# Performance work log

Measured on AMD Instinct MI355X. Metric: run time of the kernel, lower is better.

## Reference

```python
import jax, jax.numpy as jnp
import numpy as np

B = 5                      # dat_sz hardcoded in module; kernel shapes force batch == 5
X_DIM = 4096
H_DIM = 4096
T_DIM = 4096
D_DIM = X_DIM // T_DIM     # = 1 (required so z_dim == t_dim broadcasts in reparameterize_nm)
L_DIM = D_DIM * (D_DIM + 1) // 2
Z_DIM = T_DIM * L_DIM      # = 4096


def _linear_params(key, din, dout):
    kw, kb = jax.random.split(key)
    W = jax.random.normal(kw, (din, dout), dtype=jnp.float32) / np.float32(np.sqrt(din))
    b = jax.random.normal(kb, (dout,), dtype=jnp.float32) * np.float32(0.01)
    return W, b


def setup_inputs() -> dict:
    key = jax.random.key(0)
    ks = jax.random.split(key, 20)
    inp = {}
    inp["x"] = jax.random.normal(ks[0], (B, X_DIM), dtype=jnp.float32)
    inp["eps_xi"] = jax.random.normal(ks[1], (B, T_DIM), dtype=jnp.float32)
    inp["eps_f"] = jax.random.normal(ks[2], (B, D_DIM), dtype=jnp.float32)
    inp["eps_z"] = jax.random.normal(ks[3], (B, Z_DIM), dtype=jnp.float32)
    inp["W1"], inp["b1"] = _linear_params(ks[4], X_DIM, H_DIM)
    inp["W11"], inp["b11"] = _linear_params(ks[5], H_DIM, T_DIM)
    inp["W12"], inp["b12"] = _linear_params(ks[6], H_DIM, T_DIM)
    inp["W2"], inp["b2"] = _linear_params(ks[7], D_DIM, H_DIM)
    inp["W21"], inp["b21"] = _linear_params(ks[8], H_DIM, Z_DIM)
    inp["W22"], inp["b22"] = _linear_params(ks[9], H_DIM, T_DIM)
    inp["W23"], inp["b23"] = _linear_params(ks[10], X_DIM + Z_DIM, H_DIM)
    inp["W24"], inp["b24"] = _linear_params(ks[11], H_DIM, T_DIM + D_DIM)
    inp["W25"], inp["b25"] = _linear_params(ks[12], H_DIM, T_DIM + D_DIM)
    inp["W3"], inp["b3"] = _linear_params(ks[13], Z_DIM, H_DIM)
    inp["W31"], inp["b31"] = _linear_params(ks[14], H_DIM, X_DIM)
    inp["W32"], inp["b32"] = _linear_params(ks[15], H_DIM, X_DIM)
    inp["s"] = jax.random.normal(ks[16], (B, T_DIM), dtype=jnp.float32)
    inp["t"] = jax.random.normal(ks[17], (B, D_DIM), dtype=jnp.float32)
    inp["sigma"] = jnp.asarray(0.01, dtype=jnp.float32)
    inp["w"] = jnp.ones((T_DIM,), dtype=jnp.float32) / np.float32(T_DIM)
    inp["dist"] = 1  # unused by forward (matches torch signature)
    return inp


def _ard_kernel(a, b, sigma, w):
    # K[i,j] = sigma^2 * exp(-0.5 * sum_d w_d (a_i,d - b_j,d)^2)
    # Vectorized replacement of the original O(B^2) Python double loop.
    d2 = (a[:, None, :] - b[None, :, :]) ** 2            # [B, B, T]
    return (sigma ** 2) * jnp.exp(-0.5 * jnp.einsum('ijt,t->ij', d2, w))


def reference(x, eps_xi, eps_f, eps_z,
              W1, b1, W11, b11, W12, b12,
              W2, b2, W21, b21, W22, b22,
              W23, b23, W24, b24, W25, b25,
              W3, b3, W31, b31, W32, b32,
              s, t, sigma, w, dist):
    relu = jax.nn.relu
    # encode_1
    h1 = relu(x @ W1 + b1)
    qxi_mean = h1 @ W11 + b11
    log_qxi_cov = h1 @ W12 + b12
    # reparameterize_nm
    xi = jnp.exp(0.5 * log_qxi_cov) * eps_xi + qxi_mean
    # reparameterize_gp (training branch)
    K_ss = _ard_kernel(s, s, sigma, w)                    # [5,5]
    K_xs = _ard_kernel(xi, s, sigma, w)                   # [5,5]
    kk_inv = K_xs @ jnp.linalg.inv(K_ss)                  # [5,5]
    qf_mean = kk_inv @ t                                  # [5,D]
    cov = _ard_kernel(xi, xi, sigma, w) - kk_inv @ _ard_kernel(s, xi, sigma, w)
    qf_cov = jnp.diag(cov)                                # [5]
    f = jnp.sqrt(qf_cov)[:, None] * eps_f + qf_mean       # [5,D]
    # encode_2
    h2 = relu(f @ W2 + b2)
    z_mean = h2 @ W21 + b21                               # [5,Z]
    z_cov = h2 @ W22 + b22                                # [5,T] (== Z since d_dim=1)
    z = jnp.exp(0.5 * z_cov) * eps_z + z_mean
    # encode_3
    h23 = relu(jnp.concatenate([x, z], axis=1) @ W23 + b23)
    r_mean = h23 @ W24 + b24                              # [5,T+D]
    r_cov = h23 @ W25 + b25
    # decode
    h3 = relu(z @ W3 + b3)
    x_mean = h3 @ W31 + b31
    x_cov = h3 @ W32 + b32
    # losses
    qf_cov2 = jnp.broadcast_to(qf_cov[:, None], (B, D_DIM))
    q_mean = jnp.concatenate([qxi_mean, qf_mean], axis=1)
    q_cov = jnp.concatenate([log_qxi_cov, jnp.log(qf_cov2)], axis=1)
    kld1 = 0.5 * jnp.sum(-z_cov - 1.0 + jnp.exp(z_cov) + z_mean ** 2) / B
    kld2 = 0.5 * jnp.sum(r_cov - q_cov - 1.0
                         + jnp.exp(q_cov - r_cov)
                         + (q_mean - r_mean) ** 2 * jnp.exp(-r_cov)) / B
    kld_loss = kld1 + kld2
    log_pi = jnp.log(jnp.asarray(np.pi, dtype=jnp.float32))
    nll_loss = 0.5 * jnp.sum(log_pi + x_cov + jnp.exp(-x_cov) * (x - x_mean) ** 2) / B
    return (kld_loss, nll_loss, z_mean, z_cov, x_mean, x_cov)
```

## Files before the change

kernel.cpp:

```cpp
#include <hip/hip_runtime.h>
#include <math.h>

#define B5 5
#define DX 4096
#define DT 4096
#define DR 4097

enum {
  WS_SUMS  = 0,
  WS_CNT1  = 3,
  WS_CNT2  = 4,
  WS_ZERO_END = 8,
  WS_QXI_F = 16,
  WS_LQC_F = WS_QXI_F + 20480,
  WS_XIV   = WS_LQC_F + 20480,
  WS_Z     = WS_XIV   + 20480,
  WS_KSS   = WS_Z     + 20480,
  WS_KXS   = WS_KSS + 32,
  WS_F     = WS_KXS + 32,
  WS_QFM   = WS_F   + 8,
  WS_QFC   = WS_QFM + 8,
  WS_PART  = 82032,
  WS_P_H1  = WS_PART,
  WS_P_QXI = WS_P_H1  + 1310720,
  WS_P_LQC = WS_P_QXI + 1310720,
  WS_P_ZM  = WS_P_LQC + 1310720,
  WS_P_ZC  = WS_P_ZM  + 1310720,
  WS_P_H23 = WS_P_ZC  + 1310720,
  WS_P_H3  = WS_P_H23 + 2621440,
  WS_P_RM  = WS_P_H3  + 1310720,
  WS_P_RC  = WS_P_RM  + 1311040,
  WS_P_XM  = WS_P_RC  + 1311040,
  WS_P_XC  = WS_P_XM  + 1310720,
  WS_END   = WS_P_XC  + 1310720
};

#define GROWS  64
#define GBLOCK 256

__device__ inline float wave_sum(float v) {
  #pragma unroll
  for (int o = 32; o > 0; o >>= 1) v += __shfl_down(v, o, 64);
  return v;
}

__global__ void k_zero(float* __restrict__ ws)
{
  if (threadIdx.x < WS_ZERO_END) ws[threadIdx.x] = 0.f;
}

template<int PROLOG, int DUAL, int ALIGNED, int NS>
__device__ __forceinline__ void gemm5_body(
    float sx[B5][GROWS], int bx, int by,
    const float* __restrict__ p0, const float* __restrict__ p1,
    const float* __restrict__ p2,
    const float* __restrict__ Wa, const float* __restrict__ Wb,
    float* __restrict__ Pa,       float* __restrict__ Pb,
    int din, int dout)
{
  const int tid = threadIdx.x;
  const long i0 = (long)by * GROWS;

  for (int t = tid; t < B5 * GROWS; t += GBLOCK) {
    int b  = t / GROWS;
    int il = t % GROWS;
    int i  = (int)i0 + il;
    float v;
    if (PROLOG == 0)      v = p0[(long)b * din + i];
    else if (PROLOG == 2) v = fmaxf(p0[b] * p1[i] + p2[i], 0.f);
    else if (PROLOG == 3) v = (i < DX) ? p0[(long)b * DX + i] : p1[(long)b * DT + (i - DX)];
    else {
      const float* pp = p0 + (long)b * din + i;
      float acc = 0.f;
      #pragma unroll 8
      for (int ks = 0; ks < NS; ++ks) acc += pp[(long)ks * (B5 * din)];
      v = fmaxf(acc + p1[i], 0.f);
    }
    sx[b][il] = v;
  }
  __syncthreads();

  long o0 = ((long)bx * GBLOCK + tid) * 2;
  if (o0 >= dout) return;
  const bool has2 = (o0 + 1 < dout);

  float accA[B5][2] = {};
  float accB[B5][2] = {};

  const float* wa = Wa + i0 * dout + o0;
  const float* wb = DUAL ? (Wb + i0 * dout + o0) : nullptr;

  #pragma unroll 4
  for (int il = 0; il < GROWS; ++il) {
    float w0a, w1a, w0b = 0.f, w1b = 0.f;
    if (ALIGNED) {
      float2 ta = *(const float2*)wa; w0a = ta.x; w1a = ta.y;
      if (DUAL) { float2 tb = *(const float2*)wb; w0b = tb.x; w1b = tb.y; }
    } else {
      w0a = wa[0]; w1a = has2 ? wa[1] : 0.f;
      if (DUAL) { w0b = wb[0]; w1b = has2 ? wb[1] : 0.f; }
    }
    #pragma unroll
    for (int b = 0; b < B5; ++b) {
      float xv = sx[b][il];
      accA[b][0] += xv * w0a; accA[b][1] += xv * w1a;
      if (DUAL) { accB[b][0] += xv * w0b; accB[b][1] += xv * w1b; }
    }
    wa += dout; if (DUAL) wb += dout;
  }

  #pragma unroll
  for (int b = 0; b < B5; ++b) {
    float* pa = Pa + ((long)by * B5 + b) * dout + o0;
    if (ALIGNED) *(float2*)pa = make_float2(accA[b][0], accA[b][1]);
    else { pa[0] = accA[b][0]; if (has2) pa[1] = accA[b][1]; }
    if (DUAL) {
      float* pb = Pb + ((long)by * B5 + b) * dout + o0;
      if (ALIGNED) *(float2*)pb = make_float2(accB[b][0], accB[b][1]);
      else { pb[0] = accB[b][0]; if (has2) pb[1] = accB[b][1]; }
    }
  }
}

template<int PROLOG, int DUAL, int ALIGNED, int NS>
__global__ __launch_bounds__(GBLOCK) void gemm5(
    const float* __restrict__ p0, const float* __restrict__ p1,
    const float* __restrict__ p2,
    const float* __restrict__ Wa, const float* __restrict__ Wb,
    float* __restrict__ Pa,       float* __restrict__ Pb,
    int din, int dout)
{
  __shared__ float sx[B5][GROWS];
  gemm5_body<PROLOG, DUAL, ALIGNED, NS>(sx, blockIdx.x, blockIdx.y,
      p0, p1, p2, Wa, Wb, Pa, Pb, din, dout);
}

__global__ __launch_bounds__(256) void k_xi(
    const float* __restrict__ Pq, const float* __restrict__ Pl,
    const float* __restrict__ b11, const float* __restrict__ b12,
    const float* __restrict__ eps_xi,
    float* __restrict__ qf, float* __restrict__ lf, float* __restrict__ xiv)
{
  int idx = blockIdx.x * 256 + threadIdx.x;
  if (idx >= B5 * DT) return;
  int b = idx >> 12, col = idx & (DT - 1);
  const float* pq = Pq + (long)b * DT + col;
  const float* pl = Pl + (long)b * DT + col;
  float sq = 0.f, sl = 0.f;
  #pragma unroll 8
  for (int ks = 0; ks < 64; ++ks) { sq += pq[(long)ks * (B5 * DT)]; sl += pl[(long)ks * (B5 * DT)]; }
  float qm = sq + b11[col];
  float lq = sl + b12[col];
  qf[idx] = qm; lf[idx] = lq;
  xiv[idx] = expf(0.5f * lq) * eps_xi[idx] + qm;
}

__global__ __launch_bounds__(256) void k_ardgp(
    const float* __restrict__ s,    const float* __restrict__ xiv,
    const float* __restrict__ w,    const float* __restrict__ sigma,
    const float* __restrict__ t_in, const float* __restrict__ eps_f,
    float* __restrict__ Kss, float* __restrict__ Kxs, int* __restrict__ cnt,
    float* __restrict__ fv, float* __restrict__ qfm, float* __restrict__ qfc)
{
  const int bid = blockIdx.x;
  const bool xs = (bid >= 25);
  int q = xs ? bid - 25 : bid;
  const int i = q / 5, j = q % 5;
  const float* aa = xs ? (xiv + (long)i * DT) : (s + (long)i * DT);
  const float* bb = s + (long)j * DT;

  float sum = 0.f;
  for (int t = threadIdx.x; t < DT; t += 256) {
    float d = aa[t] - bb[t];
    sum += w[t] * d * d;
  }
  sum = wave_sum(sum);
  __shared__ float red[4];
  int lane = threadIdx.x & 63, wv = threadIdx.x >> 6;
  if (lane == 0) red[wv] = sum;
  __syncthreads();

  if (threadIdx.x == 0) {
    float tot = red[0] + red[1] + red[2] + red[3];
    float sg = sigma[0];
    float K = sg * sg * expf(-0.5f * tot);
    (xs ? Kxs : Kss)[i * 5 + j] = K;
    __threadfence();
    int old = atomicAdd(cnt, 1);
    if (old == 49) {
      __threadfence();
      double M[5][5], Inv[5][5];
      for (int a = 0; a < 5; ++a)
        for (int b = 0; b < 5; ++b) { M[a][b] = Kss[a * 5 + b]; Inv[a][b] = (a == b) ? 1.0 : 0.0; }
      for (int c = 0; c < 5; ++c) {
        int p = c; double best = fabs(M[c][c]);
        for (int r = c + 1; r < 5; ++r) if (fabs(M[r][c]) > best) { best = fabs(M[r][c]); p = r; }
        if (p != c)
          for (int k = 0; k < 5; ++k) {
            double tm = M[c][k]; M[c][k] = M[p][k]; M[p][k] = tm;
            tm = Inv[c][k]; Inv[c][k] = Inv[p][k]; Inv[p][k] = tm;
          }
        double piv = 1.0 / M[c][c];
        for (int k = 0; k < 5; ++k) { M[c][k] *= piv; Inv[c][k] *= piv; }
        for (int r = 0; r < 5; ++r) if (r != c) {
          double m = M[r][c];
          for (int k = 0; k < 5; ++k) { M[r][k] -= m * M[c][k]; Inv[r][k] -= m * Inv[c][k]; }
        }
      }
      double kk[5][5];
      for (int a = 0; a < 5; ++a)
        for (int b = 0; b < 5; ++b) {
          double acc = 0.0;
          for (int k = 0; k < 5; ++k) acc += (double)Kxs[a * 5 + k] * Inv[k][b];
          kk[a][b] = acc;
        }
      double sg2 = (double)sg * (double)sg;
      for (int a = 0; a < 5; ++a) {
        double qm = 0.0, qc = sg2;
        for (int b = 0; b < 5; ++b) { qm += kk[a][b] * (double)t_in[b]; qc -= kk[a][b] * (double)Kxs[a * 5 + b]; }
        if (qc < 1e-12) qc = 1e-12;
        qfm[a] = (float)qm;
        qfc[a] = (float)qc;
        fv[a]  = sqrtf((float)qc) * eps_f[a] + (float)qm;
      }
    }
  }
}

__global__ __launch_bounds__(256) void k_z(
    const float* __restrict__ Pm, const float* __restrict__ Pc,
    const float* __restrict__ b21, const float* __restrict__ b22,
    const float* __restrict__ eps_z,
    float* __restrict__ out_zm, float* __restrict__ out_zc,
    float* __restrict__ zv, float* __restrict__ kld1sum)
{
  int idx = blockIdx.x * 256 + threadIdx.x;
  float term = 0.f;
  if (idx < B5 * DT) {
    int b = idx >> 12, col = idx & (DT - 1);
    const float* pm = Pm + (long)b * DT + col;
    const float* pc = Pc + (long)b * DT + col;
    float sm = 0.f, sc = 0.f;
    #pragma unroll 8
    for (int ks = 0; ks < 64; ++ks) { sm += pm[(long)ks * (B5 * DT)]; sc += pc[(long)ks * (B5 * DT)]; }
    float zm = sm + b21[col];
    float zc = sc + b22[col];
    out_zm[idx] = zm; out_zc[idx] = zc;
    zv[idx] = expf(0.5f * zc) * eps_z[idx] + zm;
    term = -zc - 1.f + expf(zc) + zm * zm;
  }
  term = wave_sum(term);
  if ((threadIdx.x & 63) == 0) atomicAdd(kld1sum, term);
}

__global__ __launch_bounds__(256) void k_fin(
    const float* __restrict__ Prm, const float* __restrict__ Prc,
    const float* __restrict__ b24, const float* __restrict__ b25,
    const float* __restrict__ qxi, const float* __restrict__ lqc,
    const float* __restrict__ qfm, const float* __restrict__ qfc,
    const float* __restrict__ Pxm, const float* __restrict__ Pxc,
    const float* __restrict__ b31, const float* __restrict__ b32,
    const float* __restrict__ x,
    float* __restrict__ out_xm, float* __restrict__ out_xc,
    float* __restrict__ sums, int* __restrict__ cnt, float* __restrict__ out01)
{
  const int gtid = blockIdx.x * 256 + threadIdx.x;
  float t2 = 0.f, t3 = 0.f;
  if (gtid < B5 * DR) {
    int b = gtid / DR, col = gtid % DR;
    const float* pm = Prm + (long)b * DR + col;
    const float* pc = Prc + (long)b * DR + col;
    float sm = 0.f, sc = 0.f;
    #pragma unroll 8
    for (int ks = 0; ks < 64; ++ks) { sm += pm[(long)ks * (B5 * DR)]; sc += pc[(long)ks * (B5 * DR)]; }
    float rm = sm + b24[col];
    float rc = sc + b25[col];
    float qm, qc;
    if (col < DT) { qm = qxi[(long)b * DT + col]; qc = lqc[(long)b * DT + col]; }
    else          { qm = qfm[b]; qc = logf(qfc[b]); }
    float d = qm - rm;
    t2 = rc - qc - 1.f + expf(qc - rc) + d * d * expf(-rc);
  } else {
    int idx = gtid - B5 * DR;
    if (idx < B5 * DX) {
      int b = idx >> 12, col = idx & (DX - 1);
      const float* pm = Pxm + (long)b * DX + col;
      const float* pc = Pxc + (long)b * DX + col;
      float sm = 0.f, sc = 0.f;
      #pragma unroll 8
      for (int ks = 0; ks < 64; ++ks) { sm += pm[(long)ks * (B5 * DX)]; sc += pc[(long)ks * (B5 * DX)]; }
      float xm = sm + b31[col];
      float xc = sc + b32[col];
      out_xm[idx] = xm; out_xc[idx] = xc;
      float d = x[idx] - xm;
      t3 = 1.14472988584940017f + xc + expf(-xc) * d * d;
    }
  }
  t2 = wave_sum(t2);
  t3 = wave_sum(t3);
  if ((threadIdx.x & 63) == 0) {
    if (t2 != 0.f) atomicAdd(&sums[1], t2);
    if (t3 != 0.f) atomicAdd(&sums[2], t3);
  }
  __syncthreads();
  if (threadIdx.x == 0) {
    __threadfence();
    int old = atomicAdd(cnt, 1);
    if (old == (int)gridDim.x - 1) {
      __threadfence();
      out01[0] = 0.5f * (sums[0] + sums[1]) / (float)B5;
      out01[1] = 0.5f * sums[2] / (float)B5;
    }
  }
}

extern "C" void kernel_launch(void* const* d_in, const int* in_sizes, int n_in,
                              void* d_out, int out_size, void* d_ws, size_t ws_size,
                              hipStream_t stream)
{
  const float* x      = (const float*)d_in[0];
  const float* eps_xi = (const float*)d_in[1];
  const float* eps_f  = (const float*)d_in[2];
  const float* eps_z  = (const float*)d_in[3];
  const float* W1  = (const float*)d_in[4];  const float* b1  = (const float*)d_in[5];
  const float* W11 = (const float*)d_in[6];  const float* b11 = (const float*)d_in[7];
  const float* W12 = (const float*)d_in[8];  const float* b12 = (const float*)d_in[9];
  const float* W2  = (const float*)d_in[10]; const float* b2  = (const float*)d_in[11];
  const float* W21 = (const float*)d_in[12]; const float* b21 = (const float*)d_in[13];
  const float* W22 = (const float*)d_in[14]; const float* b22 = (const float*)d_in[15];
  const float* W23 = (const float*)d_in[16]; const float* b23 = (const float*)d_in[17];
  const float* W24 = (const float*)d_in[18]; const float* b24 = (const float*)d_in[19];
  const float* W25 = (const float*)d_in[20]; const float* b25 = (const float*)d_in[21];
  const float* W3  = (const float*)d_in[22]; const float* b3  = (const float*)d_in[23];
  const float* W31 = (const float*)d_in[24]; const float* b31 = (const float*)d_in[25];
  const float* W32 = (const float*)d_in[26]; const float* b32 = (const float*)d_in[27];
  const float* s     = (const float*)d_in[28];
  const float* t     = (const float*)d_in[29];
  const float* sigma = (const float*)d_in[30];
  const float* w     = (const float*)d_in[31];

  float* ws  = (float*)d_ws;
  float* out = (float*)d_out;

  dim3 blk(256);

  k_zero<<<1, 64, 0, stream>>>(ws);

  gemm5<0,0,1,1><<<dim3(8,64), blk, 0, stream>>>(
      x, nullptr, nullptr, W1, nullptr, ws + WS_P_H1, nullptr, 4096, 4096);
  gemm5<4,1,1,64><<<dim3(8,64), blk, 0, stream>>>(
      ws + WS_P_H1, b1, nullptr, W11, W12, ws + WS_P_QXI, ws + WS_P_LQC, 4096, 4096);
  k_xi<<<80, blk, 0, stream>>>(
      ws + WS_P_QXI, ws + WS_P_LQC, b11, b12, eps_xi,
      ws + WS_QXI_F, ws + WS_LQC_F, ws + WS_XIV);
  k_ardgp<<<50, blk, 0, stream>>>(
      s, ws + WS_XIV, w, sigma, t, eps_f,
      ws + WS_KSS, ws + WS_KXS, (int*)(ws + WS_CNT1),
      ws + WS_F, ws + WS_QFM, ws + WS_QFC);
  gemm5<2,1,1,1><<<dim3(8,64), blk, 0, stream>>>(
      ws + WS_F, W2, b2, W21, W22, ws + WS_P_ZM, ws + WS_P_ZC, 4096, 4096);
  k_z<<<80, blk, 0, stream>>>(
      ws + WS_P_ZM, ws + WS_P_ZC, b21, b22, eps_z,
      out + 2, out + 2 + 20480, ws + WS_Z, ws + WS_SUMS);
  gemm5<3,0,1,1><<<dim3(8,128), blk, 0, stream>>>(
      x, ws + WS_Z, nullptr, W23, nullptr, ws + WS_P_H23, nullptr, 8192, 4096);
  gemm5<4,1,0,128><<<dim3(9,64), blk, 0, stream>>>(
      ws + WS_P_H23, b23, nullptr, W24, W25, ws + WS_P_RM, ws + WS_P_RC, 4096, 4097);
  gemm5<0,0,1,1><<<dim3(8,64), blk, 0, stream>>>(
      ws + WS_Z, nullptr, nullptr, W3, nullptr, ws + WS_P_H3, nullptr, 4096, 4096);
  gemm5<4,1,1,64><<<dim3(8,64), blk, 0, stream>>>(
      ws + WS_P_H3, b3, nullptr, W31, W32, ws + WS_P_XM, ws + WS_P_XC, 4096, 4096);
  k_fin<<<161, blk, 0, stream>>>(
      ws + WS_P_RM, ws + WS_P_RC, b24, b25,
      ws + WS_QXI_F, ws + WS_LQC_F,
      ws + WS_QFM, ws + WS_QFC,
      ws + WS_P_XM, ws + WS_P_XC, b31, b32, x,
      out + 2 + 40960, out + 2 + 61440,
      ws + WS_SUMS, (int*)(ws + WS_CNT2), out);
}
```

Before: 275.3 us.

## Halve GEMV row tile and merge independent encoder/decoder GEMVs into combined launches

Halves the split-K row chunk per block from 64 to 32, doubling grid size and partial-sum buffers, so each weight-streaming GEMV has more blocks in flight. It also fuses the independent W23 and W3 GEMVs into one launch, and the W24/W25 and W31/W32 GEMVs into another, by dispatching on block index. The cost is twice as many partial sums to write and reduce in the consumer kernels, and a larger workspace.

```diff
diff --git a/kernel.cpp b/kernel.cpp
--- a/kernel.cpp
+++ b/kernel.cpp
@@ -22,20 +22,20 @@
   WS_QFC   = WS_QFM + 8,
   WS_PART  = 82032,
   WS_P_H1  = WS_PART,
-  WS_P_QXI = WS_P_H1  + 1310720,
-  WS_P_LQC = WS_P_QXI + 1310720,
-  WS_P_ZM  = WS_P_LQC + 1310720,
-  WS_P_ZC  = WS_P_ZM  + 1310720,
-  WS_P_H23 = WS_P_ZC  + 1310720,
-  WS_P_H3  = WS_P_H23 + 2621440,
-  WS_P_RM  = WS_P_H3  + 1310720,
-  WS_P_RC  = WS_P_RM  + 1311040,
-  WS_P_XM  = WS_P_RC  + 1311040,
-  WS_P_XC  = WS_P_XM  + 1310720,
-  WS_END   = WS_P_XC  + 1310720
+  WS_P_QXI = WS_P_H1  + 2621440,
+  WS_P_LQC = WS_P_QXI + 2621440,
+  WS_P_ZM  = WS_P_LQC + 2621440,
+  WS_P_ZC  = WS_P_ZM  + 2621440,
+  WS_P_H23 = WS_P_ZC  + 2621440,
+  WS_P_H3  = WS_P_H23 + 5242880,
+  WS_P_RM  = WS_P_H3  + 2621440,
+  WS_P_RC  = WS_P_RM  + 2622080,
+  WS_P_XM  = WS_P_RC  + 2622080,
+  WS_P_XC  = WS_P_XM  + 2621440,
+  WS_END   = WS_P_XC  + 2621440
 };
 
-#define GROWS  64
+#define GROWS  32
 #define GBLOCK 256
 
 __device__ inline float wave_sum(float v) {
@@ -61,9 +61,9 @@
   const int tid = threadIdx.x;
   const long i0 = (long)by * GROWS;
 
-  for (int t = tid; t < B5 * GROWS; t += GBLOCK) {
-    int b  = t / GROWS;
-    int il = t % GROWS;
+  if (tid < B5 * GROWS) {
+    int b  = tid >> 5;
+    int il = tid & 31;
     int i  = (int)i0 + il;
     float v;
     if (PROLOG == 0)      v = p0[(long)b * din + i];
@@ -90,7 +90,7 @@
   const float* wa = Wa + i0 * dout + o0;
   const float* wb = DUAL ? (Wb + i0 * dout + o0) : nullptr;
 
-  #pragma unroll 4
+  #pragma unroll 8
   for (int il = 0; il < GROWS; ++il) {
     float w0a, w1a, w0b = 0.f, w1b = 0.f;
     if (ALIGNED) {
@@ -135,6 +135,45 @@
       p0, p1, p2, Wa, Wb, Pa, Pb, din, dout);
 }
 
+#define G4_BLOCKS (8 * 256)
+__global__ __launch_bounds__(GBLOCK) void gemm5_G46(
+    const float* __restrict__ x,   const float* __restrict__ z,
+    const float* __restrict__ W23, float* __restrict__ P23,
+    const float* __restrict__ W3,  float* __restrict__ P3)
+{
+  __shared__ float sx[B5][GROWS];
+  int id = blockIdx.x;
+  if (id < G4_BLOCKS) {
+    gemm5_body<3, 0, 1, 1>(sx, id & 7, id >> 3, x, z, nullptr,
+                           W23, nullptr, P23, nullptr, 8192, 4096);
+  } else {
+    id -= G4_BLOCKS;
+    gemm5_body<0, 0, 1, 1>(sx, id & 7, id >> 3, z, nullptr, nullptr,
+                           W3, nullptr, P3, nullptr, 4096, 4096);
+  }
+}
+
+#define G5_BLOCKS (9 * 128)
+__global__ __launch_bounds__(GBLOCK) void gemm5_G57(
+    const float* __restrict__ P23, const float* __restrict__ b23,
+    const float* __restrict__ W24, const float* __restrict__ W25,
+    float* __restrict__ PRM,       float* __restrict__ PRC,
+    const float* __restrict__ P3,  const float* __restrict__ b3,
+    const float* __restrict__ W31, const float* __restrict__ W32,
+    float* __restrict__ PXM,       float* __restrict__ PXC)
+{
+  __shared__ float sx[B5][GROWS];
+  int id = blockIdx.x;
+  if (id < G5_BLOCKS) {
+    gemm5_body<4, 1, 0, 256>(sx, id % 9, id / 9, P23, b23, nullptr,
+                             W24, W25, PRM, PRC, 4096, 4097);
+  } else {
+    id -= G5_BLOCKS;
+    gemm5_body<4, 1, 1, 128>(sx, id & 7, id >> 3, P3, b3, nullptr,
+                             W31, W32, PXM, PXC, 4096, 4096);
+  }
+}
+
 __global__ __launch_bounds__(256) void k_xi(
     const float* __restrict__ Pq, const float* __restrict__ Pl,
     const float* __restrict__ b11, const float* __restrict__ b12,
@@ -148,7 +187,7 @@
   const float* pl = Pl + (long)b * DT + col;
   float sq = 0.f, sl = 0.f;
   #pragma unroll 8
-  for (int ks = 0; ks < 64; ++ks) { sq += pq[(long)ks * (B5 * DT)]; sl += pl[(long)ks * (B5 * DT)]; }
+  for (int ks = 0; ks < 128; ++ks) { sq += pq[(long)ks * (B5 * DT)]; sl += pl[(long)ks * (B5 * DT)]; }
   float qm = sq + b11[col];
   float lq = sl + b12[col];
   qf[idx] = qm; lf[idx] = lq;
@@ -242,7 +281,7 @@
     const float* pc = Pc + (long)b * DT + col;
     float sm = 0.f, sc = 0.f;
     #pragma unroll 8
-    for (int ks = 0; ks < 64; ++ks) { sm += pm[(long)ks * (B5 * DT)]; sc += pc[(long)ks * (B5 * DT)]; }
+    for (int ks = 0; ks < 128; ++ks) { sm += pm[(long)ks * (B5 * DT)]; sc += pc[(long)ks * (B5 * DT)]; }
     float zm = sm + b21[col];
     float zc = sc + b22[col];
     out_zm[idx] = zm; out_zc[idx] = zc;
@@ -272,7 +311,7 @@
     const float* pc = Prc + (long)b * DR + col;
     float sm = 0.f, sc = 0.f;
     #pragma unroll 8
-    for (int ks = 0; ks < 64; ++ks) { sm += pm[(long)ks * (B5 * DR)]; sc += pc[(long)ks * (B5 * DR)]; }
+    for (int ks = 0; ks < 128; ++ks) { sm += pm[(long)ks * (B5 * DR)]; sc += pc[(long)ks * (B5 * DR)]; }
     float rm = sm + b24[col];
     float rc = sc + b25[col];
     float qm, qc;
@@ -288,7 +327,7 @@
       const float* pc = Pxc + (long)b * DX + col;
       float sm = 0.f, sc = 0.f;
       #pragma unroll 8
-      for (int ks = 0; ks < 64; ++ks) { sm += pm[(long)ks * (B5 * DX)]; sc += pc[(long)ks * (B5 * DX)]; }
+      for (int ks = 0; ks < 128; ++ks) { sm += pm[(long)ks * (B5 * DX)]; sc += pc[(long)ks * (B5 * DX)]; }
       float xm = sm + b31[col];
       float xc = sc + b32[col];
       out_xm[idx] = xm; out_xc[idx] = xc;
@@ -346,9 +385,9 @@
 
   k_zero<<<1, 64, 0, stream>>>(ws);
 
-  gemm5<0,0,1,1><<<dim3(8,64), blk, 0, stream>>>(
+  gemm5<0,0,1,1><<<dim3(8,128), blk, 0, stream>>>(
       x, nullptr, nullptr, W1, nullptr, ws + WS_P_H1, nullptr, 4096, 4096);
-  gemm5<4,1,1,64><<<dim3(8,64), blk, 0, stream>>>(
+  gemm5<4,1,1,128><<<dim3(8,128), blk, 0, stream>>>(
       ws + WS_P_H1, b1, nullptr, W11, W12, ws + WS_P_QXI, ws + WS_P_LQC, 4096, 4096);
   k_xi<<<80, blk, 0, stream>>>(
       ws + WS_P_QXI, ws + WS_P_LQC, b11, b12, eps_xi,
@@ -357,19 +396,16 @@
       s, ws + WS_XIV, w, sigma, t, eps_f,
       ws + WS_KSS, ws + WS_KXS, (int*)(ws + WS_CNT1),
       ws + WS_F, ws + WS_QFM, ws + WS_QFC);
-  gemm5<2,1,1,1><<<dim3(8,64), blk, 0, stream>>>(
+  gemm5<2,1,1,1><<<dim3(8,128), blk, 0, stream>>>(
       ws + WS_F, W2, b2, W21, W22, ws + WS_P_ZM, ws + WS_P_ZC, 4096, 4096);
   k_z<<<80, blk, 0, stream>>>(
       ws + WS_P_ZM, ws + WS_P_ZC, b21, b22, eps_z,
       out + 2, out + 2 + 20480, ws + WS_Z, ws + WS_SUMS);
-  gemm5<3,0,1,1><<<dim3(8,128), blk, 0, stream>>>(
-      x, ws + WS_Z, nullptr, W23, nullptr, ws + WS_P_H23, nullptr, 8192, 4096);
-  gemm5<4,1,0,128><<<dim3(9,64), blk, 0, stream>>>(
-      ws + WS_P_H23, b23, nullptr, W24, W25, ws + WS_P_RM, ws + WS_P_RC, 4096, 4097);
-  gemm5<0,0,1,1><<<dim3(8,64), blk, 0, stream>>>(
-      ws + WS_Z, nullptr, nullptr, W3, nullptr, ws + WS_P_H3, nullptr, 4096, 4096);
-  gemm5<4,1,1,64><<<dim3(8,64), blk, 0, stream>>>(
-      ws + WS_P_H3, b3, nullptr, W31, W32, ws + WS_P_XM, ws + WS_P_XC, 4096, 4096);
+  gemm5_G46<<<G4_BLOCKS + 8 * 128, blk, 0, stream>>>(
+      x, ws + WS_Z, W23, ws + WS_P_H23, W3, ws + WS_P_H3);
+  gemm5_G57<<<G5_BLOCKS + 8 * 128, blk, 0, stream>>>(
+      ws + WS_P_H23, b23, W24, W25, ws + WS_P_RM, ws + WS_P_RC,
+      ws + WS_P_H3,  b3,  W31, W32, ws + WS_P_XM, ws + WS_P_XC);
   k_fin<<<161, blk, 0, stream>>>(
       ws + WS_P_RM, ws + WS_P_RC, b24, b25,
       ws + WS_QXI_F, ws + WS_LQC_F,
```

Measured after the change: 354.3 us. 28.7% more time.

## Split GEMV tiles across waves, precompute activations, and merge independent GEMVs into combined launches

Applied to the files above, without the earlier changes.

Each block now covers 128 output columns, and its four waves each take 16 of the block's 64 input rows, combining their partial sums through shared memory. This gives four times as many blocks and a shorter per-thread loop. The split-K reduction of the hidden activations moves out of each GEMM prolog into small dedicated kernels (k_act1, k_act23), so it is no longer recomputed in every block. Independent GEMMs (W23 with W3, and W24/W25 with W31/W32) are fused into single launches to cut launch count and improve occupancy. The cost is extra shared-memory reduction steps, barriers and additional small kernels.

```diff
diff --git a/kernel.cpp b/kernel.cpp
--- a/kernel.cpp
+++ b/kernel.cpp
@@ -11,7 +11,10 @@
   WS_CNT1  = 3,
   WS_CNT2  = 4,
   WS_ZERO_END = 8,
-  WS_QXI_F = 16,
+  WS_ACT1  = 16,
+  WS_ACT23 = WS_ACT1  + 20480,
+  WS_ACT3  = WS_ACT23 + 20480,
+  WS_QXI_F = WS_ACT3  + 20480,
   WS_LQC_F = WS_QXI_F + 20480,
   WS_XIV   = WS_LQC_F + 20480,
   WS_Z     = WS_XIV   + 20480,
@@ -20,7 +23,7 @@
   WS_F     = WS_KXS + 32,
   WS_QFM   = WS_F   + 8,
   WS_QFC   = WS_QFM + 8,
-  WS_PART  = 82032,
+  WS_PART  = 143472,
   WS_P_H1  = WS_PART,
   WS_P_QXI = WS_P_H1  + 1310720,
   WS_P_LQC = WS_P_QXI + 1310720,
@@ -35,8 +38,9 @@
   WS_END   = WS_P_XC  + 1310720
 };
 
-#define GROWS  64
-#define GBLOCK 256
+#define GCOLS 128
+#define GK    64
+#define WROWS 16
 
 __device__ inline float wave_sum(float v) {
   #pragma unroll
@@ -49,90 +53,196 @@
   if (threadIdx.x < WS_ZERO_END) ws[threadIdx.x] = 0.f;
 }
 
-template<int PROLOG, int DUAL, int ALIGNED, int NS>
+template<int PROLOG, int DUAL, int ALIGNED>
 __device__ __forceinline__ void gemm5_body(
-    float sx[B5][GROWS], int bx, int by,
+    float* sx, float* red, int bx, int by,
     const float* __restrict__ p0, const float* __restrict__ p1,
     const float* __restrict__ p2,
     const float* __restrict__ Wa, const float* __restrict__ Wb,
     float* __restrict__ Pa,       float* __restrict__ Pb,
     int din, int dout)
 {
-  const int tid = threadIdx.x;
-  const long i0 = (long)by * GROWS;
-
-  for (int t = tid; t < B5 * GROWS; t += GBLOCK) {
-    int b  = t / GROWS;
-    int il = t % GROWS;
+  const int tid  = threadIdx.x;
+  const int lane = tid & 63;
+  const int wv   = tid >> 6;
+  const long i0  = (long)by * GK;
+
+  for (int t = tid; t < B5 * GK; t += 256) {
+    int b  = t >> 6;
+    int il = t & 63;
     int i  = (int)i0 + il;
     float v;
     if (PROLOG == 0)      v = p0[(long)b * din + i];
     else if (PROLOG == 2) v = fmaxf(p0[b] * p1[i] + p2[i], 0.f);
-    else if (PROLOG == 3) v = (i < DX) ? p0[(long)b * DX + i] : p1[(long)b * DT + (i - DX)];
-    else {
-      const float* pp = p0 + (long)b * din + i;
-      float acc = 0.f;
-      #pragma unroll 8
-      for (int ks = 0; ks < NS; ++ks) acc += pp[(long)ks * (B5 * din)];
-      v = fmaxf(acc + p1[i], 0.f);
-    }
-    sx[b][il] = v;
-  }
-  __syncthreads();
-
-  long o0 = ((long)bx * GBLOCK + tid) * 2;
-  if (o0 >= dout) return;
-  const bool has2 = (o0 + 1 < dout);
+    else                  v = (i < DX) ? p0[(long)b * DX + i] : p1[(long)b * DT + (i - DX)];
+    sx[b * GK + il] = v;
+  }
+  __syncthreads();
+
+  const long o0 = (long)bx * GCOLS + lane * 2;
+  const bool v0 = (o0 < dout);
+  const bool v1 = (o0 + 1 < dout);
 
   float accA[B5][2] = {};
   float accB[B5][2] = {};
-
-  const float* wa = Wa + i0 * dout + o0;
-  const float* wb = DUAL ? (Wb + i0 * dout + o0) : nullptr;
+  const long r0 = i0 + (long)wv * WROWS;
+  const float* wa = Wa + r0 * dout + o0;
+  const float* wb = DUAL ? (Wb + r0 * dout + o0) : nullptr;
 
   #pragma unroll 4
-  for (int il = 0; il < GROWS; ++il) {
+  for (int il = 0; il < WROWS; ++il) {
     float w0a, w1a, w0b = 0.f, w1b = 0.f;
     if (ALIGNED) {
       float2 ta = *(const float2*)wa; w0a = ta.x; w1a = ta.y;
       if (DUAL) { float2 tb = *(const float2*)wb; w0b = tb.x; w1b = tb.y; }
     } else {
-      w0a = wa[0]; w1a = has2 ? wa[1] : 0.f;
-      if (DUAL) { w0b = wb[0]; w1b = has2 ? wb[1] : 0.f; }
-    }
-    #pragma unroll
-    for (int b = 0; b < B5; ++b) {
-      float xv = sx[b][il];
+      w0a = v0 ? wa[0] : 0.f; w1a = v1 ? wa[1] : 0.f;
+      if (DUAL) { w0b = v0 ? wb[0] : 0.f; w1b = v1 ? wb[1] : 0.f; }
+    }
+    #pragma unroll
+    for (int b = 0; b < B5; ++b) {
+      float xv = sx[b * GK + wv * WROWS + il];
       accA[b][0] += xv * w0a; accA[b][1] += xv * w1a;
       if (DUAL) { accB[b][0] += xv * w0b; accB[b][1] += xv * w1b; }
     }
     wa += dout; if (DUAL) wb += dout;
   }
 
-  #pragma unroll
-  for (int b = 0; b < B5; ++b) {
-    float* pa = Pa + ((long)by * B5 + b) * dout + o0;
-    if (ALIGNED) *(float2*)pa = make_float2(accA[b][0], accA[b][1]);
-    else { pa[0] = accA[b][0]; if (has2) pa[1] = accA[b][1]; }
-    if (DUAL) {
-      float* pb = Pb + ((long)by * B5 + b) * dout + o0;
-      if (ALIGNED) *(float2*)pb = make_float2(accB[b][0], accB[b][1]);
-      else { pb[0] = accB[b][0]; if (has2) pb[1] = accB[b][1]; }
-    }
-  }
-}
-
-template<int PROLOG, int DUAL, int ALIGNED, int NS>
-__global__ __launch_bounds__(GBLOCK) void gemm5(
+  const int NJ = DUAL ? 20 : 10;
+  if (wv >= 2) {
+    float* rr = red + (long)(wv - 2) * NJ * 64 + lane;
+    #pragma unroll
+    for (int b = 0; b < B5; ++b) {
+      rr[(b*2)*64] = accA[b][0]; rr[(b*2+1)*64] = accA[b][1];
+      if (DUAL) { rr[(10+b*2)*64] = accB[b][0]; rr[(10+b*2+1)*64] = accB[b][1]; }
+    }
+  }
+  __syncthreads();
+  if (wv < 2) {
+    const float* rr = red + (long)wv * NJ * 64 + lane;
+    #pragma unroll
+    for (int b = 0; b < B5; ++b) {
+      accA[b][0] += rr[(b*2)*64]; accA[b][1] += rr[(b*2+1)*64];
+      if (DUAL) { accB[b][0] += rr[(10+b*2)*64]; accB[b][1] += rr[(10+b*2+1)*64]; }
+    }
+  }
+  __syncthreads();
+  if (wv == 1) {
+    float* rr = red + lane;
+    #pragma unroll
+    for (int b = 0; b < B5; ++b) {
+      rr[(b*2)*64] = accA[b][0]; rr[(b*2+1)*64] = accA[b][1];
+      if (DUAL) { rr[(10+b*2)*64] = accB[b][0]; rr[(10+b*2+1)*64] = accB[b][1]; }
+    }
+  }
+  __syncthreads();
+  if (wv == 0 && v0) {
+    const float* rr = red + lane;
+    #pragma unroll
+    for (int b = 0; b < B5; ++b) {
+      accA[b][0] += rr[(b*2)*64]; accA[b][1] += rr[(b*2+1)*64];
+      if (DUAL) { accB[b][0] += rr[(10+b*2)*64]; accB[b][1] += rr[(10+b*2+1)*64]; }
+    }
+    #pragma unroll
+    for (int b = 0; b < B5; ++b) {
+      float* pa = Pa + ((long)by * B5 + b) * dout + o0;
+      if (ALIGNED) *(float2*)pa = make_float2(accA[b][0], accA[b][1]);
+      else { pa[0] = accA[b][0]; if (v1) pa[1] = accA[b][1]; }
+      if (DUAL) {
+        float* pb = Pb + ((long)by * B5 + b) * dout + o0;
+        if (ALIGNED) *(float2*)pb = make_float2(accB[b][0], accB[b][1]);
+        else { pb[0] = accB[b][0]; if (v1) pb[1] = accB[b][1]; }
+      }
+    }
+  }
+}
+
+template<int PROLOG, int DUAL, int ALIGNED>
+__global__ __launch_bounds__(256) void gemm5(
     const float* __restrict__ p0, const float* __restrict__ p1,
     const float* __restrict__ p2,
     const float* __restrict__ Wa, const float* __restrict__ Wb,
     float* __restrict__ Pa,       float* __restrict__ Pb,
     int din, int dout)
 {
-  __shared__ float sx[B5][GROWS];
-  gemm5_body<PROLOG, DUAL, ALIGNED, NS>(sx, blockIdx.x, blockIdx.y,
+  __shared__ float sx[B5 * GK];
+  __shared__ float red[2 * 20 * 64];
+  gemm5_body<PROLOG, DUAL, ALIGNED>(sx, red, blockIdx.x, blockIdx.y,
       p0, p1, p2, Wa, Wb, Pa, Pb, din, dout);
+}
+
+__global__ __launch_bounds__(256) void gemm5_G46(
+    const float* __restrict__ x,   const float* __restrict__ z,
+    const float* __restrict__ W23, float* __restrict__ P23,
+    const float* __restrict__ W3,  float* __restrict__ P3)
+{
+  __shared__ float sx[B5 * GK];
+  __shared__ float red[2 * 20 * 64];
+  int id = blockIdx.x;
+  if (id < 4096) {
+    gemm5_body<3, 0, 1>(sx, red, id & 31, id >> 5, x, z, nullptr,
+                        W23, nullptr, P23, nullptr, 8192, 4096);
+  } else {
+    id -= 4096;
+    gemm5_body<0, 0, 1>(sx, red, id & 31, id >> 5, z, nullptr, nullptr,
+                        W3, nullptr, P3, nullptr, 4096, 4096);
+  }
+}
+
+__global__ __launch_bounds__(256) void gemm5_G57(
+    const float* __restrict__ act23,
+    const float* __restrict__ W24, const float* __restrict__ W25,
+    float* __restrict__ PRM,       float* __restrict__ PRC,
+    const float* __restrict__ act3,
+    const float* __restrict__ W31, const float* __restrict__ W32,
+    float* __restrict__ PXM,       float* __restrict__ PXC)
+{
+  __shared__ float sx[B5 * GK];
+  __shared__ float red[2 * 20 * 64];
+  int id = blockIdx.x;
+  if (id < 2112) {
+    gemm5_body<0, 1, 0>(sx, red, id % 33, id / 33, act23, nullptr, nullptr,
+                        W24, W25, PRM, PRC, 4096, 4097);
+  } else {
+    id -= 2112;
+    gemm5_body<0, 1, 1>(sx, red, id & 31, id >> 5, act3, nullptr, nullptr,
+                        W31, W32, PXM, PXC, 4096, 4096);
+  }
+}
+
+__global__ __launch_bounds__(256) void k_act1(
+    const float* __restrict__ P, const float* __restrict__ bias, float* __restrict__ act)
+{
+  int idx = blockIdx.x * 256 + threadIdx.x;
+  int b = idx >> 12, col = idx & (DT - 1);
+  const float* pp = P + (long)b * DT + col;
+  float s = 0.f;
+  #pragma unroll 8
+  for (int ks = 0; ks < 64; ++ks) s += pp[(long)ks * (B5 * DT)];
+  act[idx] = fmaxf(s + bias[col], 0.f);
+}
+
+__global__ __launch_bounds__(256) void k_act23(
+    const float* __restrict__ P23, const float* __restrict__ b23, float* __restrict__ act23,
+    const float* __restrict__ P3,  const float* __restrict__ b3,  float* __restrict__ act3)
+{
+  int idx = blockIdx.x * 256 + threadIdx.x;
+  if (idx < B5 * DT) {
+    int b = idx >> 12, col = idx & (DT - 1);
+    const float* pp = P23 + (long)b * DT + col;
+    float s = 0.f;
+    #pragma unroll 8
+    for (int ks = 0; ks < 128; ++ks) s += pp[(long)ks * (B5 * DT)];
+    act23[idx] = fmaxf(s + b23[col], 0.f);
+  } else {
+    int j = idx - B5 * DT;
+    int b = j >> 12, col = j & (DT - 1);
+    const float* pp = P3 + (long)b * DT + col;
+    float s = 0.f;
+    #pragma unroll 8
+    for (int ks = 0; ks < 64; ++ks) s += pp[(long)ks * (B5 * DT)];
+    act3[j] = fmaxf(s + b3[col], 0.f);
+  }
 }
 
 __global__ __launch_bounds__(256) void k_xi(
@@ -346,10 +456,11 @@
 
   k_zero<<<1, 64, 0, stream>>>(ws);
 
-  gemm5<0,0,1,1><<<dim3(8,64), blk, 0, stream>>>(
+  gemm5<0,0,1><<<dim3(32,64), blk, 0, stream>>>(
       x, nullptr, nullptr, W1, nullptr, ws + WS_P_H1, nullptr, 4096, 4096);
-  gemm5<4,1,1,64><<<dim3(8,64), blk, 0, stream>>>(
-      ws + WS_P_H1, b1, nullptr, W11, W12, ws + WS_P_QXI, ws + WS_P_LQC, 4096, 4096);
+  k_act1<<<80, blk, 0, stream>>>(ws + WS_P_H1, b1, ws + WS_ACT1);
+  gemm5<0,1,1><<<dim3(32,64), blk, 0, stream>>>(
+      ws + WS_ACT1, nullptr, nullptr, W11, W12, ws + WS_P_QXI, ws + WS_P_LQC, 4096, 4096);
   k_xi<<<80, blk, 0, stream>>>(
       ws + WS_P_QXI, ws + WS_P_LQC, b11, b12, eps_xi,
       ws + WS_QXI_F, ws + WS_LQC_F, ws + WS_XIV);
@@ -357,19 +468,18 @@
       s, ws + WS_XIV, w, sigma, t, eps_f,
       ws + WS_KSS, ws + WS_KXS, (int*)(ws + WS_CNT1),
       ws + WS_F, ws + WS_QFM, ws + WS_QFC);
-  gemm5<2,1,1,1><<<dim3(8,64), blk, 0, stream>>>(
+  gemm5<2,1,1><<<dim3(32,64), blk, 0, stream>>>(
       ws + WS_F, W2, b2, W21, W22, ws + WS_P_ZM, ws + WS_P_ZC, 4096, 4096);
   k_z<<<80, blk, 0, stream>>>(
       ws + WS_P_ZM, ws + WS_P_ZC, b21, b22, eps_z,
       out + 2, out + 2 + 20480, ws + WS_Z, ws + WS_SUMS);
-  gemm5<3,0,1,1><<<dim3(8,128), blk, 0, stream>>>(
-      x, ws + WS_Z, nullptr, W23, nullptr, ws + WS_P_H23, nullptr, 8192, 4096);
-  gemm5<4,1,0,128><<<dim3(9,64), blk, 0, stream>>>(
-      ws + WS_P_H23, b23, nullptr, W24, W25, ws + WS_P_RM, ws + WS_P_RC, 4096, 4097);
-  gemm5<0,0,1,1><<<dim3(8,64), blk, 0, stream>>>(
-      ws + WS_Z, nullptr, nullptr, W3, nullptr, ws + WS_P_H3, nullptr, 4096, 4096);
-  gemm5<4,1,1,64><<<dim3(8,64), blk, 0, stream>>>(
-      ws + WS_P_H3, b3, nullptr, W31, W32, ws + WS_P_XM, ws + WS_P_XC, 4096, 4096);
+  gemm5_G46<<<6144, blk, 0, stream>>>(
+      x, ws + WS_Z, W23, ws + WS_P_H23, W3, ws + WS_P_H3);
+  k_act23<<<160, blk, 0, stream>>>(
+      ws + WS_P_H23, b23, ws + WS_ACT23, ws + WS_P_H3, b3, ws + WS_ACT3);
+  gemm5_G57<<<4160, blk, 0, stream>>>(
+      ws + WS_ACT23, W24, W25, ws + WS_P_RM, ws + WS_P_RC,
+      ws + WS_ACT3,  W31, W32, ws + WS_P_XM, ws + WS_P_XC);
   k_fin<<<161, blk, 0, stream>>>(
       ws + WS_P_RM, ws + WS_P_RC, b24, b25,
       ws + WS_QXI_F, ws + WS_LQC_F,
```

Measured after the change: 248.1 us. 1.11x faster.
